# Kernel optimization log

Hardware: AMD Instinct MI355X
Metric: run time of the kernel (lower is better)

The kernel has to match this reference:

```python
import jax, jax.numpy as jnp
import numpy as np

NUM_HEADS = 12

def setup_inputs() -> dict:
    key = jax.random.key(0)
    ks = jax.random.split(key, 6)
    B, N, C = 16, 1024, 768
    H, d = NUM_HEADS, C // NUM_HEADS
    return {
        "x": jax.random.normal(ks[0], (B, N, C), dtype=jnp.float32),
        "W_qkv": jax.random.normal(ks[1], (C, 3 * C), dtype=jnp.float32) * 0.02,
        "b_qkv": jax.random.normal(ks[2], (3 * C,), dtype=jnp.float32) * 0.02,
        "zeta": jnp.ones((1, 1, H, 1, d), dtype=jnp.float32),
        "W_proj": jax.random.normal(ks[3], (C, C), dtype=jnp.float32) * 0.02,
        "b_proj": jax.random.normal(ks[4], (C,), dtype=jnp.float32) * 0.02,
        "mask": jnp.zeros((B, N), dtype=bool),
    }

def reference(x, W_qkv, b_qkv, zeta, W_proj, b_proj, mask):
    B, N, C = x.shape
    H = NUM_HEADS
    d = C // H
    scale = d ** -0.5
    # qkv: (B,N,3C) -> (B,N,3,H,d) -> (3,B,H,N,d), gated by zeta (1,1,H,1,d)
    qkv = (x @ W_qkv + b_qkv).reshape(B, N, 3, H, d).transpose(2, 0, 3, 1, 4)
    qkv = qkv * zeta
    q, k, v = qkv[0], qkv[1], qkv[2]
    attn = jnp.einsum("bhnd,bhmd->bhnm", q, k) * scale
    # mask (B,N) over keys -> (B,1,1,N)
    attn = jnp.where(mask[:, None, None, :], -jnp.inf, attn)
    attn = jax.nn.softmax(attn, axis=-1)
    out = jnp.einsum("bhnm,bhmd->bhnd", attn, v)          # (B,H,N,d)
    out = out.transpose(0, 2, 1, 3).reshape(B, N, C)
    return out @ W_proj + b_proj
```

## Files before the change

### kernel.cpp

```cpp
#include <hip/hip_runtime.h>
#include <hip/hip_bf16.h>

typedef unsigned short ushort_t;
typedef __bf16 bf16_t;
typedef bf16_t bf16x8 __attribute__((ext_vector_type(8)));
typedef float floatx4 __attribute__((ext_vector_type(4)));
typedef ushort_t ushortx8 __attribute__((ext_vector_type(8)));

struct alignas(8) us4 { ushort_t x, y, z, w; };

__device__ __forceinline__ ushort_t f2bf(float f) {
  union { float f; unsigned int u; } v; v.f = f;
  unsigned int u = v.u;
  return (ushort_t)((u + 0x7fffu + ((u >> 16) & 1u)) >> 16);
}

__device__ __forceinline__ unsigned int pk_bf16(float a, float b) {
  __hip_bfloat162 h = __float22bfloat162_rn(float2{a, b});
  union { __hip_bfloat162 h; unsigned int u; } v; v.h = h;
  return v.u;
}

__device__ __forceinline__ void async16(const void* g, void* l) {
  __builtin_amdgcn_global_load_lds(
      (const __attribute__((address_space(1))) unsigned int*)g,
      (__attribute__((address_space(3))) unsigned int*)l, 16, 0, 0);
}

#define LOG2E 1.44269504088896340736f


__global__ __launch_bounds__(256) void k_cvt_x(const float* __restrict__ in,
                                               ushort_t* __restrict__ out) {
  size_t i = ((size_t)blockIdx.x * 256 + threadIdx.x) * 8;
  float4 a = *(const float4*)(in + i);
  float4 b = *(const float4*)(in + i + 4);
  ushortx8 o;
  o[0] = f2bf(a.x); o[1] = f2bf(a.y); o[2] = f2bf(a.z); o[3] = f2bf(a.w);
  o[4] = f2bf(b.x); o[5] = f2bf(b.y); o[6] = f2bf(b.z); o[7] = f2bf(b.w);
  *(ushortx8*)(out + i) = o;
}

__global__ __launch_bounds__(256) void k_transpose_bf16(const float* __restrict__ in,
                                                        ushort_t* __restrict__ out,
                                                        int R, int C) {
  __shared__ float tile[32][33];
  int c0 = blockIdx.x * 32, r0 = blockIdx.y * 32;
  int tx = threadIdx.x, ty = threadIdx.y;
#pragma unroll
  for (int i = 0; i < 32; i += 8)
    tile[ty + i][tx] = in[(size_t)(r0 + ty + i) * C + c0 + tx];
  __syncthreads();
#pragma unroll
  for (int i = 0; i < 32; i += 8)
    out[(size_t)(c0 + ty + i) * R + r0 + tx] = f2bf(tile[tx][ty + i]);
}


__device__ __forceinline__ void gemm_bt_mainloop(const ushort_t* __restrict__ A,
                                                 const ushort_t* __restrict__ Bt,
                                                 int m0, int n0,
                                                 ushort_t* sA, ushort_t* sB,
                                                 floatx4 acc[4][4]) {
  const int t = threadIdx.x;
  const int lane = t & 63, w = t >> 6;
  const int wr = w >> 1, wc = w & 1;
  const int lr = lane & 15, qd = lane >> 4;
  const int swz = ((t & 3) ^ ((t >> 3) & 3)) * 8;
  const ushort_t* gA = A + (size_t)(m0 + (t >> 2)) * 768 + swz;
  const ushort_t* gB = Bt + (size_t)(n0 + (t >> 2)) * 768 + swz;
  char* lA = (char*)sA + t * 16;
  char* lB = (char*)sB + t * 16;
  const int rsz = (qd ^ ((lr >> 1) & 3)) * 16;
  for (int k0 = 0; k0 < 768; k0 += 32) {
    __syncthreads();
    async16(gA + k0, lA);
    async16(gA + k0 + 64 * 768, lA + 4096);
    async16(gB + k0, lB);
    async16(gB + k0 + 64 * 768, lB + 4096);
    asm volatile("s_waitcnt vmcnt(0)" ::: "memory");
    __syncthreads();
    bf16x8 af[4], bfr[4];
#pragma unroll
    for (int i = 0; i < 4; ++i)
      af[i] = *(const bf16x8*)((const char*)sA + (wr * 64 + i * 16 + lr) * 64 + rsz);
#pragma unroll
    for (int j = 0; j < 4; ++j)
      bfr[j] = *(const bf16x8*)((const char*)sB + (wc * 64 + j * 16 + lr) * 64 + rsz);
#pragma unroll
    for (int i = 0; i < 4; ++i)
#pragma unroll
      for (int j = 0; j < 4; ++j)
        acc[i][j] = __builtin_amdgcn_mfma_f32_16x16x32_bf16(af[i], bfr[j], acc[i][j], 0, 0, 0);
  }
}


__global__ __launch_bounds__(256) void k_qkv(const ushort_t* __restrict__ xb,
                                             const ushort_t* __restrict__ WqT,
                                             const float* __restrict__ bqkv,
                                             const float* __restrict__ zeta,
                                             ushort_t* __restrict__ qb,
                                             ushort_t* __restrict__ kb,
                                             ushort_t* __restrict__ vtb) {
  __shared__ alignas(16) ushort_t sA[128 * 32];
  __shared__ alignas(16) ushort_t sB[128 * 32];
  floatx4 acc[4][4] = {};
  const int m0 = blockIdx.y * 128, n0 = blockIdx.x * 128;
  gemm_bt_mainloop(xb, WqT, m0, n0, sA, sB, acc);
  const int t = threadIdx.x, lane = t & 63, w = t >> 6;
  const int wr = w >> 1, wc = w & 1, lr = lane & 15, qd = lane >> 4;
  const int tq = n0 / 768;
#pragma unroll
  for (int j = 0; j < 4; ++j) {
    int n = n0 + wc * 64 + j * 16 + lr;
    int nc = n - tq * 768;
    int h = nc >> 6, dim = n & 63;
    float bias = bqkv[n];
    float zv = zeta[nc];
    float mult = (tq == 0) ? zv * 0.125f * LOG2E : zv;
    if (tq < 2) {
      ushort_t* dst = (tq == 0) ? qb : kb;
#pragma unroll
      for (int i = 0; i < 4; ++i) {
        int mbase = m0 + wr * 64 + i * 16 + qd * 4;
#pragma unroll
        for (int r = 0; r < 4; ++r) {
          int m = mbase + r;
          int b = m >> 10, seq = m & 1023;
          dst[(((size_t)b * 12 + h) * 1024 + seq) * 64 + dim] = f2bf((acc[i][j][r] + bias) * mult);
        }
      }
    } else {
#pragma unroll
      for (int i = 0; i < 4; ++i) {
        int mbase = m0 + wr * 64 + i * 16 + qd * 4;
        int b = mbase >> 10, seq = mbase & 1023;
        us4 pk;
        pk.x = f2bf((acc[i][j][0] + bias) * mult);
        pk.y = f2bf((acc[i][j][1] + bias) * mult);
        pk.z = f2bf((acc[i][j][2] + bias) * mult);
        pk.w = f2bf((acc[i][j][3] + bias) * mult);
        *(us4*)&vtb[(((size_t)b * 12 + h) * 64 + dim) * 1024 + seq] = pk;
      }
    }
  }
}


__global__ __launch_bounds__(256, 3) void k_attn(const ushort_t* __restrict__ qg,
                                                 const ushort_t* __restrict__ kg,
                                                 const ushort_t* __restrict__ vg,
                                                 const unsigned char* __restrict__ mask,
                                                 ushort_t* __restrict__ ob) {
  __shared__ alignas(16) char smem[49664];
  char* sV = smem + 32768;
  float* maskadd = (float*)(smem + 49152);
  const int t = threadIdx.x, lane = t & 63, w = t >> 6;
  const int lr = lane & 15, qd = lane >> 4;
  const int lin = blockIdx.x;
  const int bh = (lin & 7) + 8 * (lin >> 6);
  const int qt = (lin >> 3) & 7;
  const int b = bh / 12, h = bh % 12;
  const int qrow0 = qt * 128 + w * 32;
  const ushort_t* qp = qg + (size_t)bh * 65536;
  const ushort_t* kp = kg + (size_t)bh * 65536;
  const ushort_t* vp = vg + (size_t)bh * 65536;
  const unsigned char* mp = mask + b * 1024;

  bf16x8 qf[2][2];
#pragma unroll
  for (int ns = 0; ns < 2; ++ns)
#pragma unroll
    for (int kk = 0; kk < 2; ++kk)
      qf[ns][kk] = *(const bf16x8*)(qp + (size_t)(qrow0 + ns * 16 + lr) * 64 + kk * 32 + qd * 8);

  floatx4 o[4][2] = {};
  float lst[2] = {0.f, 0.f};
  char* sPw = smem + 16384 + w * 4096;

  for (int kt = 0; kt < 8; ++kt) {
    __syncthreads();
    const ushort_t* kpt = kp + kt * 8192;
#pragma unroll
    for (int it = 0; it < 4; ++it) {
      int p = it * 256 + t;
      int r = p >> 3, cs = (p & 7) ^ (r & 7);
      async16(kpt + r * 64 + cs * 8, smem + p * 16);
    }
    const ushort_t* vpt = vp + kt * 128;
#pragma unroll
    for (int it = 0; it < 4; ++it) {
      int p = it * 256 + t;
      int r = p >> 4, cs = (p & 15) ^ (r & 15);
      async16(vpt + (size_t)r * 1024 + cs * 8, sV + p * 16);
    }
    if (t < 128) maskadd[t] = mp[kt * 128 + t] ? -1e30f : 0.0f;
    asm volatile("s_waitcnt vmcnt(0)" ::: "memory");
    __syncthreads();

#pragma unroll
    for (int hh = 0; hh < 2; ++hh) {
      floatx4 s[4][2] = {};
#pragma unroll
      for (int kk = 0; kk < 2; ++kk) {
#pragma unroll
        for (int ms = 0; ms < 4; ++ms) {
          bf16x8 ak = *(const bf16x8*)(smem + ((hh * 4 + ms) * 16 + lr) * 128 +
                                       ((kk * 4 + qd) ^ (lr & 7)) * 16);
#pragma unroll
          for (int ns = 0; ns < 2; ++ns)
            s[ms][ns] = __builtin_amdgcn_mfma_f32_16x16x32_bf16(ak, qf[ns][kk], s[ms][ns], 0, 0, 0);
        }
      }
#pragma unroll
      for (int ms = 0; ms < 4; ++ms) {
        float4 mk = *(const float4*)&maskadd[(hh * 4 + ms) * 16 + qd * 4];
#pragma unroll
        for (int ns = 0; ns < 2; ++ns) {
          float p0 = __builtin_amdgcn_exp2f(s[ms][ns][0] + mk.x);
          float p1 = __builtin_amdgcn_exp2f(s[ms][ns][1] + mk.y);
          float p2 = __builtin_amdgcn_exp2f(s[ms][ns][2] + mk.z);
          float p3 = __builtin_amdgcn_exp2f(s[ms][ns][3] + mk.w);
          lst[ns] += (p0 + p1) + (p2 + p3);
          uint2 pk;
          pk.x = pk_bf16(p0, p1);
          pk.y = pk_bf16(p2, p3);
          *(uint2*)(sPw + (ns * 16 + lr) * 128 +
                    ((ms * 2 + (qd >> 1)) ^ (lr & 7)) * 16 + (qd & 1) * 8) = pk;
        }
      }
      asm volatile("s_waitcnt lgkmcnt(0)" ::: "memory");
#pragma unroll
      for (int kk = 0; kk < 2; ++kk) {
        bf16x8 pb[2];
#pragma unroll
        for (int ns = 0; ns < 2; ++ns)
          pb[ns] = *(const bf16x8*)(sPw + (ns * 16 + lr) * 128 +
                                    ((kk * 4 + qd) ^ (lr & 7)) * 16);
#pragma unroll
        for (int ds = 0; ds < 4; ++ds) {
          bf16x8 av = *(const bf16x8*)(sV + (ds * 16 + lr) * 256 +
                                       ((hh * 8 + kk * 4 + qd) ^ lr) * 16);
#pragma unroll
          for (int ns = 0; ns < 2; ++ns)
            o[ds][ns] = __builtin_amdgcn_mfma_f32_16x16x32_bf16(av, pb[ns], o[ds][ns], 0, 0, 0);
        }
      }
    }
  }
#pragma unroll
  for (int ns = 0; ns < 2; ++ns) {
    lst[ns] += __shfl_xor(lst[ns], 16);
    lst[ns] += __shfl_xor(lst[ns], 32);
  }
#pragma unroll
  for (int ns = 0; ns < 2; ++ns) {
    float rl = 1.0f / lst[ns];
    size_t row = (size_t)(b * 1024 + qrow0 + ns * 16 + lr) * 768 + h * 64;
#pragma unroll
    for (int ds = 0; ds < 4; ++ds) {
      uint2 ov;
      ov.x = pk_bf16(o[ds][ns][0] * rl, o[ds][ns][1] * rl);
      ov.y = pk_bf16(o[ds][ns][2] * rl, o[ds][ns][3] * rl);
      *(uint2*)&ob[row + ds * 16 + qd * 4] = ov;
    }
  }
}


__global__ __launch_bounds__(256) void k_proj(const ushort_t* __restrict__ ob,
                                              const ushort_t* __restrict__ WpT,
                                              const float* __restrict__ bproj,
                                              float* __restrict__ out) {
  __shared__ alignas(16) ushort_t sA[128 * 32];
  __shared__ alignas(16) ushort_t sB[128 * 32];
  floatx4 acc[4][4] = {};
  const int m0 = blockIdx.y * 128, n0 = blockIdx.x * 128;
  gemm_bt_mainloop(ob, WpT, m0, n0, sA, sB, acc);
  const int t = threadIdx.x, lane = t & 63, w = t >> 6;
  const int wr = w >> 1, wc = w & 1, lr = lane & 15, qd = lane >> 4;
#pragma unroll
  for (int j = 0; j < 4; ++j) {
    int n = n0 + wc * 64 + j * 16 + lr;
    float bias = bproj[n];
#pragma unroll
    for (int i = 0; i < 4; ++i) {
      int mbase = m0 + wr * 64 + i * 16 + qd * 4;
#pragma unroll
      for (int r = 0; r < 4; ++r)
        out[(size_t)(mbase + r) * 768 + n] = acc[i][j][r] + bias;
    }
  }
}


extern "C" void kernel_launch(void* const* d_in, const int* in_sizes, int n_in,
                              void* d_out, int out_size, void* d_ws, size_t ws_size,
                              hipStream_t stream) {
  const float* x = (const float*)d_in[0];
  const float* bqkv = (const float*)d_in[2];
  const float* zeta = (const float*)d_in[3];
  const float* bproj = (const float*)d_in[5];
  const unsigned char* mask = (const unsigned char*)d_in[6];
  float* out = (float*)d_out;
  char* ws = (char*)d_ws;
  ushort_t* xb  = (ushort_t*)(ws);
  ushort_t* WqT = (ushort_t*)(ws + 25165824);
  ushort_t* WpT = (ushort_t*)(ws + 28704768);
  ushort_t* qb  = (ushort_t*)(ws + 29884416);
  ushort_t* kb  = (ushort_t*)(ws + 55050240);
  ushort_t* vtb = (ushort_t*)(ws + 80216064);
  ushort_t* ob  = xb;

  k_cvt_x<<<dim3(6144), dim3(256), 0, stream>>>(x, xb);
  k_transpose_bf16<<<dim3(72, 24), dim3(32, 8), 0, stream>>>((const float*)d_in[1], WqT, 768, 2304);
  k_transpose_bf16<<<dim3(24, 24), dim3(32, 8), 0, stream>>>((const float*)d_in[4], WpT, 768, 768);
  k_qkv<<<dim3(18, 128), dim3(256), 0, stream>>>(xb, WqT, bqkv, zeta, qb, kb, vtb);
  k_attn<<<dim3(1536), dim3(256), 0, stream>>>(qb, kb, vtb, mask, ob);
  k_proj<<<dim3(6, 128), dim3(256), 0, stream>>>(ob, WpT, bproj, out);
}
```

Baseline: 313.6 us.

## Double-buffer GEMM mainloop and merge prep kernels into one launch

Replaces the single-buffer GEMM mainloop with a double-buffered LDS pipeline, so the async global-to-LDS loads for the next K tile overlap the MFMA work on the current one. It also adds an occupancy hint of 4 blocks to the QKV and projection kernels. The x conversion and both weight transposes are merged into one prep kernel, saving two launches. LDS use per block doubles, which could limit occupancy, and the waitcnt plus barrier still sits at the end of every iteration.

Result: faster. 307.4 us (-2.0%).

```diff
diff --git a/kernel.cpp b/kernel.cpp
--- a/kernel.cpp
+++ b/kernel.cpp
@@ -30,38 +30,50 @@
 #define LOG2E 1.44269504088896340736f
 
 
-__global__ __launch_bounds__(256) void k_cvt_x(const float* __restrict__ in,
-                                               ushort_t* __restrict__ out) {
-  size_t i = ((size_t)blockIdx.x * 256 + threadIdx.x) * 8;
-  float4 a = *(const float4*)(in + i);
-  float4 b = *(const float4*)(in + i + 4);
-  ushortx8 o;
-  o[0] = f2bf(a.x); o[1] = f2bf(a.y); o[2] = f2bf(a.z); o[3] = f2bf(a.w);
-  o[4] = f2bf(b.x); o[5] = f2bf(b.y); o[6] = f2bf(b.z); o[7] = f2bf(b.w);
-  *(ushortx8*)(out + i) = o;
-}
-
-__global__ __launch_bounds__(256) void k_transpose_bf16(const float* __restrict__ in,
-                                                        ushort_t* __restrict__ out,
-                                                        int R, int C) {
+__global__ __launch_bounds__(256) void k_prep(const float* __restrict__ x,
+                                              ushort_t* __restrict__ xb,
+                                              const float* __restrict__ Wq,
+                                              ushort_t* __restrict__ WqT,
+                                              const float* __restrict__ Wp,
+                                              ushort_t* __restrict__ WpT) {
   __shared__ float tile[32][33];
-  int c0 = blockIdx.x * 32, r0 = blockIdx.y * 32;
-  int tx = threadIdx.x, ty = threadIdx.y;
+  const int bid = blockIdx.x, t = threadIdx.x;
+  if (bid < 6144) {
+    size_t i = ((size_t)bid * 256 + t) * 8;
+    float4 a = *(const float4*)(x + i);
+    float4 b = *(const float4*)(x + i + 4);
+    ushortx8 o;
+    o[0] = f2bf(a.x); o[1] = f2bf(a.y); o[2] = f2bf(a.z); o[3] = f2bf(a.w);
+    o[4] = f2bf(b.x); o[5] = f2bf(b.y); o[6] = f2bf(b.z); o[7] = f2bf(b.w);
+    *(ushortx8*)(xb + i) = o;
+    return;
+  }
+  const float* in; ushort_t* out; int C, c0, r0;
+  if (bid < 7872) {
+    int b2 = bid - 6144;
+    in = Wq; out = WqT; C = 2304;
+    c0 = (b2 % 72) * 32; r0 = (b2 / 72) * 32;
+  } else {
+    int b3 = bid - 7872;
+    in = Wp; out = WpT; C = 768;
+    c0 = (b3 % 24) * 32; r0 = (b3 / 24) * 32;
+  }
+  const int tx = t & 31, ty = t >> 5;
 #pragma unroll
   for (int i = 0; i < 32; i += 8)
     tile[ty + i][tx] = in[(size_t)(r0 + ty + i) * C + c0 + tx];
   __syncthreads();
 #pragma unroll
   for (int i = 0; i < 32; i += 8)
-    out[(size_t)(c0 + ty + i) * R + r0 + tx] = f2bf(tile[tx][ty + i]);
-}
-
-
-__device__ __forceinline__ void gemm_bt_mainloop(const ushort_t* __restrict__ A,
-                                                 const ushort_t* __restrict__ Bt,
-                                                 int m0, int n0,
-                                                 ushort_t* sA, ushort_t* sB,
-                                                 floatx4 acc[4][4]) {
+    out[(size_t)(c0 + ty + i) * 768 + r0 + tx] = f2bf(tile[tx][ty + i]);
+}
+
+
+__device__ __forceinline__ void gemm_bt_dbuf(const ushort_t* __restrict__ A,
+                                             const ushort_t* __restrict__ Bt,
+                                             int m0, int n0,
+                                             ushort_t* sA, ushort_t* sB,
+                                             floatx4 acc[4][4]) {
   const int t = threadIdx.x;
   const int lane = t & 63, w = t >> 6;
   const int wr = w >> 1, wc = w & 1;
@@ -72,42 +84,54 @@
   char* lA = (char*)sA + t * 16;
   char* lB = (char*)sB + t * 16;
   const int rsz = (qd ^ ((lr >> 1) & 3)) * 16;
-  for (int k0 = 0; k0 < 768; k0 += 32) {
-    __syncthreads();
-    async16(gA + k0, lA);
-    async16(gA + k0 + 64 * 768, lA + 4096);
-    async16(gB + k0, lB);
-    async16(gB + k0 + 64 * 768, lB + 4096);
+  async16(gA, lA);
+  async16(gA + 64 * 768, lA + 4096);
+  async16(gB, lB);
+  async16(gB + 64 * 768, lB + 4096);
+  asm volatile("s_waitcnt vmcnt(0)" ::: "memory");
+  __syncthreads();
+#pragma unroll 2
+  for (int k = 0; k < 24; ++k) {
+    const int p = k & 1, pn = p ^ 1;
+    if (k < 23) {
+      const int k0 = (k + 1) * 32;
+      async16(gA + k0, lA + pn * 8192);
+      async16(gA + k0 + 64 * 768, lA + pn * 8192 + 4096);
+      async16(gB + k0, lB + pn * 8192);
+      async16(gB + k0 + 64 * 768, lB + pn * 8192 + 4096);
+    }
+    const char* cA = (const char*)sA + p * 8192;
+    const char* cB = (const char*)sB + p * 8192;
+    bf16x8 af[4], bfr[4];
+#pragma unroll
+    for (int i = 0; i < 4; ++i)
+      af[i] = *(const bf16x8*)(cA + (wr * 64 + i * 16 + lr) * 64 + rsz);
+#pragma unroll
+    for (int j = 0; j < 4; ++j)
+      bfr[j] = *(const bf16x8*)(cB + (wc * 64 + j * 16 + lr) * 64 + rsz);
+#pragma unroll
+    for (int i = 0; i < 4; ++i)
+#pragma unroll
+      for (int j = 0; j < 4; ++j)
+        acc[i][j] = __builtin_amdgcn_mfma_f32_16x16x32_bf16(af[i], bfr[j], acc[i][j], 0, 0, 0);
     asm volatile("s_waitcnt vmcnt(0)" ::: "memory");
     __syncthreads();
-    bf16x8 af[4], bfr[4];
-#pragma unroll
-    for (int i = 0; i < 4; ++i)
-      af[i] = *(const bf16x8*)((const char*)sA + (wr * 64 + i * 16 + lr) * 64 + rsz);
-#pragma unroll
-    for (int j = 0; j < 4; ++j)
-      bfr[j] = *(const bf16x8*)((const char*)sB + (wc * 64 + j * 16 + lr) * 64 + rsz);
-#pragma unroll
-    for (int i = 0; i < 4; ++i)
-#pragma unroll
-      for (int j = 0; j < 4; ++j)
-        acc[i][j] = __builtin_amdgcn_mfma_f32_16x16x32_bf16(af[i], bfr[j], acc[i][j], 0, 0, 0);
-  }
-}
-
-
-__global__ __launch_bounds__(256) void k_qkv(const ushort_t* __restrict__ xb,
-                                             const ushort_t* __restrict__ WqT,
-                                             const float* __restrict__ bqkv,
-                                             const float* __restrict__ zeta,
-                                             ushort_t* __restrict__ qb,
-                                             ushort_t* __restrict__ kb,
-                                             ushort_t* __restrict__ vtb) {
-  __shared__ alignas(16) ushort_t sA[128 * 32];
-  __shared__ alignas(16) ushort_t sB[128 * 32];
+  }
+}
+
+
+__global__ __launch_bounds__(256, 4) void k_qkv(const ushort_t* __restrict__ xb,
+                                                const ushort_t* __restrict__ WqT,
+                                                const float* __restrict__ bqkv,
+                                                const float* __restrict__ zeta,
+                                                ushort_t* __restrict__ qb,
+                                                ushort_t* __restrict__ kb,
+                                                ushort_t* __restrict__ vtb) {
+  __shared__ alignas(16) ushort_t sA[2 * 128 * 32];
+  __shared__ alignas(16) ushort_t sB[2 * 128 * 32];
   floatx4 acc[4][4] = {};
   const int m0 = blockIdx.y * 128, n0 = blockIdx.x * 128;
-  gemm_bt_mainloop(xb, WqT, m0, n0, sA, sB, acc);
+  gemm_bt_dbuf(xb, WqT, m0, n0, sA, sB, acc);
   const int t = threadIdx.x, lane = t & 63, w = t >> 6;
   const int wr = w >> 1, wc = w & 1, lr = lane & 15, qd = lane >> 4;
   const int tq = n0 / 768;
@@ -269,15 +293,15 @@
 }
 
 
-__global__ __launch_bounds__(256) void k_proj(const ushort_t* __restrict__ ob,
-                                              const ushort_t* __restrict__ WpT,
-                                              const float* __restrict__ bproj,
-                                              float* __restrict__ out) {
-  __shared__ alignas(16) ushort_t sA[128 * 32];
-  __shared__ alignas(16) ushort_t sB[128 * 32];
+__global__ __launch_bounds__(256, 4) void k_proj(const ushort_t* __restrict__ ob,
+                                                 const ushort_t* __restrict__ WpT,
+                                                 const float* __restrict__ bproj,
+                                                 float* __restrict__ out) {
+  __shared__ alignas(16) ushort_t sA[2 * 128 * 32];
+  __shared__ alignas(16) ushort_t sB[2 * 128 * 32];
   floatx4 acc[4][4] = {};
   const int m0 = blockIdx.y * 128, n0 = blockIdx.x * 128;
-  gemm_bt_mainloop(ob, WpT, m0, n0, sA, sB, acc);
+  gemm_bt_dbuf(ob, WpT, m0, n0, sA, sB, acc);
   const int t = threadIdx.x, lane = t & 63, w = t >> 6;
   const int wr = w >> 1, wc = w & 1, lr = lane & 15, qd = lane >> 4;
 #pragma unroll
@@ -313,9 +337,8 @@
   ushort_t* vtb = (ushort_t*)(ws + 80216064);
   ushort_t* ob  = xb;
 
-  k_cvt_x<<<dim3(6144), dim3(256), 0, stream>>>(x, xb);
-  k_transpose_bf16<<<dim3(72, 24), dim3(32, 8), 0, stream>>>((const float*)d_in[1], WqT, 768, 2304);
-  k_transpose_bf16<<<dim3(24, 24), dim3(32, 8), 0, stream>>>((const float*)d_in[4], WpT, 768, 768);
+  k_prep<<<dim3(8448), dim3(256), 0, stream>>>(x, xb, (const float*)d_in[1], WqT,
+                                               (const float*)d_in[4], WpT);
   k_qkv<<<dim3(18, 128), dim3(256), 0, stream>>>(xb, WqT, bqkv, zeta, qb, kb, vtb);
   k_attn<<<dim3(1536), dim3(256), 0, stream>>>(qb, kb, vtb, mask, ob);
   k_proj<<<dim3(6, 128), dim3(256), 0, stream>>>(ob, WpT, bproj, out);
```
